# Optimization experiments

Hardware: AMD Instinct MI355X
Metric: run time of the kernel (lower is better)

## Reference

```python
import jax, jax.numpy as jnp
import numpy as np

EPS = 1e-06


def setup_inputs() -> dict:
    key = jax.random.key(0)
    kx, kw, kb = jax.random.split(key, 3)
    C = 128
    x = jax.random.normal(kx, (8, C, 256, 256), dtype=jnp.float32)
    # 1x1 conv weights: [C_out, C_in]
    W = jax.random.normal(kw, (C, C), dtype=jnp.float32) * (1.0 / np.sqrt(C))
    b = jax.random.normal(kb, (C,), dtype=jnp.float32) * 0.01
    return {"x": x, "W": W, "b": b}


def reference(x, W, b):
    # torch.std_mean over channel dim (dim=1), std is unbiased (ddof=1)
    u = jnp.mean(x, axis=1, keepdims=True)                  # [B,1,H,W]
    var = jnp.var(x, axis=1, keepdims=True, ddof=1)         # unbiased
    s = jnp.sqrt(var)
    n_x = (x - u) / (s + EPS)
    # 1x1 conv == pointwise GEMM over channels
    n_x = jnp.einsum('bchw,oc->bohw', n_x, W) + b[None, :, None, None]
    return x * n_x
```

## Files before the change

kernel.cpp:

```cpp
#include <hip/hip_runtime.h>

#define EPS 1e-6f

constexpr int C    = 128;
constexpr int HW   = 65536;
constexpr int TILE = 128;
constexpr int NT   = 512;

typedef __attribute__((ext_vector_type(8))) short bf16x8;
typedef __attribute__((ext_vector_type(4))) float f32x4;

__device__ __forceinline__ unsigned short f2bf(float f) {
    unsigned u = __float_as_uint(f);
    u += 0x7fff + ((u >> 16) & 1);
    return (unsigned short)(u >> 16);
}
__device__ __forceinline__ float bf2f(unsigned short u) {
    return __uint_as_float(((unsigned)u) << 16);
}
__device__ __forceinline__ unsigned pack2(float lo, float hi) {
    return (unsigned)f2bf(lo) | ((unsigned)f2bf(hi) << 16);
}

__global__ __launch_bounds__(NT, 4) void spnorm_kernel(
    const float* __restrict__ x, const float* __restrict__ W,
    const float* __restrict__ bias, float* __restrict__ out)
{
    __shared__ unsigned short buf[TILE * C];
    __shared__ float red1[4][TILE], red2[4][TILE];
    __shared__ float u_s[TILE], iv_s[TILE], se_s[TILE];

    const int tid  = threadIdx.x;
    const int l    = tid & 63;
    const int wv   = tid >> 6;
    const int batch = blockIdx.x >> 9;
    const int hw0   = (blockIdx.x & 511) * TILE;
    const int base  = batch * (C * HW) + hw0;

    const int arow  = (wv << 4) + (l & 15);
    const int acol0 = (l >> 4) << 3;
    bf16x8 afrag[4];
    #pragma unroll
    for (int kk = 0; kk < 4; ++kk) {
        const float* wp = W + arow * C + kk * 32 + acol0;
        float4 wa = *reinterpret_cast<const float4*>(wp);
        float4 wb = *reinterpret_cast<const float4*>(wp + 4);
        bf16x8 f;
        f[0] = (short)f2bf(wa.x); f[1] = (short)f2bf(wa.y);
        f[2] = (short)f2bf(wa.z); f[3] = (short)f2bf(wa.w);
        f[4] = (short)f2bf(wb.x); f[5] = (short)f2bf(wb.y);
        f[6] = (short)f2bf(wb.z); f[7] = (short)f2bf(wb.w);
        afrag[kk] = f;
    }
    const int od = (wv << 4) + ((l >> 4) << 2);
    const f32x4 binit = { bias[od], bias[od + 1], bias[od + 2], bias[od + 3] };

    {
        unsigned short* nb = buf;
        #pragma unroll
        for (int it = 0; it < 8; ++it) {
            int i4 = it * NT + tid;
            int c  = i4 >> 5;
            int p4 = (i4 & 31) << 2;
            float4 v = *reinterpret_cast<const float4*>(x + base + c * HW + p4);
            uint2 d;
            d.x = pack2(v.x, v.y);
            d.y = pack2(v.z, v.w);
            *reinterpret_cast<uint2*>(&nb[c * TILE + p4]) = d;
        }
    }
    __syncthreads();

    const int p = tid & 127;
    const int q = tid >> 7;
    float v[32];
    {
        const unsigned short* nb = buf;
        float s1 = 0.f, s2 = 0.f;
        #pragma unroll
        for (int i = 0; i < 32; ++i) {
            float t = bf2f(nb[(q * 32 + i) * TILE + p]);
            v[i] = t;
            s1 += t;
            s2 = fmaf(t, t, s2);
        }
        red1[q][p] = s1;
        red2[q][p] = s2;
    }
    __syncthreads();
    if (tid < TILE) {
        float s1 = red1[0][tid] + red1[1][tid] + red1[2][tid] + red1[3][tid];
        float s2 = red2[0][tid] + red2[1][tid] + red2[2][tid] + red2[3][tid];
        float u   = s1 * (1.0f / 128.0f);
        float var = fmaxf((s2 - s1 * u) * (1.0f / 127.0f), 0.0f);
        float se  = sqrtf(var) + EPS;
        u_s[tid]  = u;
        se_s[tid] = se;
        iv_s[tid] = 1.0f / se;
    }
    __syncthreads();

    {
        char* nbTc = (char*)buf;
        const float u  = u_s[p];
        const float iv = iv_s[p];
        const int rowoff = p * 256;
        const int swz    = (p & 15) << 4;
        #pragma unroll
        for (int o8 = 0; o8 < 4; ++o8) {
            float n0 = (v[o8 * 8 + 0] - u) * iv;
            float n1 = (v[o8 * 8 + 1] - u) * iv;
            float n2 = (v[o8 * 8 + 2] - u) * iv;
            float n3 = (v[o8 * 8 + 3] - u) * iv;
            float n4 = (v[o8 * 8 + 4] - u) * iv;
            float n5 = (v[o8 * 8 + 5] - u) * iv;
            float n6 = (v[o8 * 8 + 6] - u) * iv;
            float n7 = (v[o8 * 8 + 7] - u) * iv;
            uint4 d;
            d.x = pack2(n0, n1);
            d.y = pack2(n2, n3);
            d.z = pack2(n4, n5);
            d.w = pack2(n6, n7);
            int byte = (rowoff + (q * 4 + o8) * 16) ^ swz;
            *reinterpret_cast<uint4*>(nbTc + byte) = d;
        }
    }
    __syncthreads();

    {
        const char* nbTc = (const char*)buf;
        const int pcol = l & 15;
        const int koff = (l >> 4) << 4;
        const int swz  = pcol << 4;
        float* outp = out + base;
        #pragma unroll
        for (int pt = 0; pt < 8; ++pt) {
            const int pp     = (pt << 4) + pcol;
            const int rowoff = pp * 256;
            f32x4 acc = binit;
            #pragma unroll
            for (int kk = 0; kk < 4; ++kk) {
                int byte = (rowoff + kk * 64 + koff) ^ swz;
                bf16x8 bfrag = *reinterpret_cast<const bf16x8*>(nbTc + byte);
                acc = __builtin_amdgcn_mfma_f32_16x16x32_bf16(afrag[kk], bfrag, acc, 0, 0, 0);
            }
            const float uu = u_s[pp];
            const float se = se_s[pp];
            int nbyte = (rowoff + od * 2) ^ swz;
            uint2 nn = *reinterpret_cast<const uint2*>(nbTc + nbyte);
            float x0 = fmaf(bf2f((unsigned short)(nn.x & 0xffffu)), se, uu);
            float x1 = fmaf(bf2f((unsigned short)(nn.x >> 16)),     se, uu);
            float x2 = fmaf(bf2f((unsigned short)(nn.y & 0xffffu)), se, uu);
            float x3 = fmaf(bf2f((unsigned short)(nn.y >> 16)),     se, uu);
            outp[(od + 0) * HW + pp] = x0 * acc[0];
            outp[(od + 1) * HW + pp] = x1 * acc[1];
            outp[(od + 2) * HW + pp] = x2 * acc[2];
            outp[(od + 3) * HW + pp] = x3 * acc[3];
        }
    }
}

extern "C" void kernel_launch(void* const* d_in, const int* in_sizes, int n_in,
                              void* d_out, int out_size, void* d_ws, size_t ws_size,
                              hipStream_t stream) {
    const float* x = (const float*)d_in[0];
    const float* W = (const float*)d_in[1];
    const float* b = (const float*)d_in[2];
    float* out     = (float*)d_out;

    const int nblk = 8 * HW / TILE;
    spnorm_kernel<<<nblk, NT, 0, stream>>>(x, W, b, out);
}
```

Baseline: 123.4 us.

## Loop each block over eight tiles with register prefetch of the next tile

Each block now processes eight consecutive 128-pixel tiles instead of one, so the grid shrinks eightfold. The next tile's global loads are issued into registers at the start of each iteration and written into a separate LDS input buffer after the normalization stage, overlapping global load latency with the reduction, normalize and MFMA work. A second LDS buffer holds the transposed normalized tile, and full __syncthreads are replaced by lgkmcnt waits plus raw barriers. The larger LDS footprint and the 32 prefetch registers may reduce resident blocks per CU, and the smaller grid leaves less parallelism to hide memory latency.

```diff
diff --git a/kernel.cpp b/kernel.cpp
--- a/kernel.cpp
+++ b/kernel.cpp
@@ -2,10 +2,11 @@
 
 #define EPS 1e-6f
 
-constexpr int C    = 128;
-constexpr int HW   = 65536;
-constexpr int TILE = 128;
-constexpr int NT   = 512;
+constexpr int C      = 128;
+constexpr int HW     = 65536;
+constexpr int TILE   = 128;
+constexpr int NT     = 512;
+constexpr int NTILES = 8;
 
 typedef __attribute__((ext_vector_type(8))) short bf16x8;
 typedef __attribute__((ext_vector_type(4))) float f32x4;
@@ -22,20 +23,34 @@
     return (unsigned)f2bf(lo) | ((unsigned)f2bf(hi) << 16);
 }
 
+#define BAR() do { \
+    asm volatile("s_waitcnt lgkmcnt(0)" ::: "memory"); \
+    __builtin_amdgcn_s_barrier(); \
+    __builtin_amdgcn_sched_barrier(0); \
+} while (0)
+
 __global__ __launch_bounds__(NT, 4) void spnorm_kernel(
     const float* __restrict__ x, const float* __restrict__ W,
     const float* __restrict__ bias, float* __restrict__ out)
 {
-    __shared__ unsigned short buf[TILE * C];
+    __shared__ unsigned short bufN[C * TILE];
+    __shared__ unsigned short bufT[C * TILE];
     __shared__ float red1[4][TILE], red2[4][TILE];
     __shared__ float u_s[TILE], iv_s[TILE], se_s[TILE];
 
-    const int tid  = threadIdx.x;
-    const int l    = tid & 63;
-    const int wv   = tid >> 6;
-    const int batch = blockIdx.x >> 9;
-    const int hw0   = (blockIdx.x & 511) * TILE;
-    const int base  = batch * (C * HW) + hw0;
+    const int tid = threadIdx.x;
+    const int l   = tid & 63;
+    const int wv  = tid >> 6;
+
+    const int blkPerImg = HW / (TILE * NTILES);
+    const int batch = blockIdx.x / blkPerImg;
+    const int hw0   = (blockIdx.x % blkPerImg) * (TILE * NTILES);
+    const int ibase = batch * (C * HW) + hw0;
+
+    const int sc  = tid >> 5;
+    const int sp4 = (tid & 31) << 2;
+    const int p = tid & 127;
+    const int q = tid >> 7;
 
     const int arow  = (wv << 4) + (l & 15);
     const int acol0 = (l >> 4) << 3;
@@ -56,106 +71,120 @@
     const f32x4 binit = { bias[od], bias[od + 1], bias[od + 2], bias[od + 3] };
 
     {
-        unsigned short* nb = buf;
+        const float* xb = x + ibase;
         #pragma unroll
         for (int it = 0; it < 8; ++it) {
-            int i4 = it * NT + tid;
-            int c  = i4 >> 5;
-            int p4 = (i4 & 31) << 2;
-            float4 v = *reinterpret_cast<const float4*>(x + base + c * HW + p4);
+            float4 v = *reinterpret_cast<const float4*>(xb + (it * 16 + sc) * HW + sp4);
             uint2 d;
             d.x = pack2(v.x, v.y);
             d.y = pack2(v.z, v.w);
-            *reinterpret_cast<uint2*>(&nb[c * TILE + p4]) = d;
+            *reinterpret_cast<uint2*>(&bufN[(it * 16 + sc) * TILE + sp4]) = d;
         }
     }
-    __syncthreads();
-
-    const int p = tid & 127;
-    const int q = tid >> 7;
-    float v[32];
-    {
-        const unsigned short* nb = buf;
-        float s1 = 0.f, s2 = 0.f;
-        #pragma unroll
-        for (int i = 0; i < 32; ++i) {
-            float t = bf2f(nb[(q * 32 + i) * TILE + p]);
-            v[i] = t;
-            s1 += t;
-            s2 = fmaf(t, t, s2);
-        }
-        red1[q][p] = s1;
-        red2[q][p] = s2;
-    }
-    __syncthreads();
-    if (tid < TILE) {
-        float s1 = red1[0][tid] + red1[1][tid] + red1[2][tid] + red1[3][tid];
-        float s2 = red2[0][tid] + red2[1][tid] + red2[2][tid] + red2[3][tid];
-        float u   = s1 * (1.0f / 128.0f);
-        float var = fmaxf((s2 - s1 * u) * (1.0f / 127.0f), 0.0f);
-        float se  = sqrtf(var) + EPS;
-        u_s[tid]  = u;
-        se_s[tid] = se;
-        iv_s[tid] = 1.0f / se;
-    }
-    __syncthreads();
-
-    {
-        char* nbTc = (char*)buf;
-        const float u  = u_s[p];
-        const float iv = iv_s[p];
-        const int rowoff = p * 256;
-        const int swz    = (p & 15) << 4;
-        #pragma unroll
-        for (int o8 = 0; o8 < 4; ++o8) {
-            float n0 = (v[o8 * 8 + 0] - u) * iv;
-            float n1 = (v[o8 * 8 + 1] - u) * iv;
-            float n2 = (v[o8 * 8 + 2] - u) * iv;
-            float n3 = (v[o8 * 8 + 3] - u) * iv;
-            float n4 = (v[o8 * 8 + 4] - u) * iv;
-            float n5 = (v[o8 * 8 + 5] - u) * iv;
-            float n6 = (v[o8 * 8 + 6] - u) * iv;
-            float n7 = (v[o8 * 8 + 7] - u) * iv;
-            uint4 d;
-            d.x = pack2(n0, n1);
-            d.y = pack2(n2, n3);
-            d.z = pack2(n4, n5);
-            d.w = pack2(n6, n7);
-            int byte = (rowoff + (q * 4 + o8) * 16) ^ swz;
-            *reinterpret_cast<uint4*>(nbTc + byte) = d;
-        }
-    }
-    __syncthreads();
-
-    {
-        const char* nbTc = (const char*)buf;
-        const int pcol = l & 15;
-        const int koff = (l >> 4) << 4;
-        const int swz  = pcol << 4;
-        float* outp = out + base;
-        #pragma unroll
-        for (int pt = 0; pt < 8; ++pt) {
-            const int pp     = (pt << 4) + pcol;
-            const int rowoff = pp * 256;
-            f32x4 acc = binit;
-            #pragma unroll
-            for (int kk = 0; kk < 4; ++kk) {
-                int byte = (rowoff + kk * 64 + koff) ^ swz;
-                bf16x8 bfrag = *reinterpret_cast<const bf16x8*>(nbTc + byte);
-                acc = __builtin_amdgcn_mfma_f32_16x16x32_bf16(afrag[kk], bfrag, acc, 0, 0, 0);
-            }
-            const float uu = u_s[pp];
-            const float se = se_s[pp];
-            int nbyte = (rowoff + od * 2) ^ swz;
-            uint2 nn = *reinterpret_cast<const uint2*>(nbTc + nbyte);
-            float x0 = fmaf(bf2f((unsigned short)(nn.x & 0xffffu)), se, uu);
-            float x1 = fmaf(bf2f((unsigned short)(nn.x >> 16)),     se, uu);
-            float x2 = fmaf(bf2f((unsigned short)(nn.y & 0xffffu)), se, uu);
-            float x3 = fmaf(bf2f((unsigned short)(nn.y >> 16)),     se, uu);
-            outp[(od + 0) * HW + pp] = x0 * acc[0];
-            outp[(od + 1) * HW + pp] = x1 * acc[1];
-            outp[(od + 2) * HW + pp] = x2 * acc[2];
-            outp[(od + 3) * HW + pp] = x3 * acc[3];
+    BAR();
+
+    for (int t = 0; t < NTILES; ++t) {
+        float4 pf[8];
+        if (t + 1 < NTILES) {
+            const float* xb = x + ibase + (t + 1) * TILE;
+            #pragma unroll
+            for (int it = 0; it < 8; ++it)
+                pf[it] = *reinterpret_cast<const float4*>(xb + (it * 16 + sc) * HW + sp4);
+        }
+
+        float v[32];
+        {
+            float s1 = 0.f, s2 = 0.f;
+            #pragma unroll
+            for (int i = 0; i < 32; ++i) {
+                float tv = bf2f(bufN[(q * 32 + i) * TILE + p]);
+                v[i] = tv;
+                s1 += tv;
+                s2 = fmaf(tv, tv, s2);
+            }
+            red1[q][p] = s1;
+            red2[q][p] = s2;
+        }
+        BAR();
+        if (tid < TILE) {
+            float s1 = red1[0][tid] + red1[1][tid] + red1[2][tid] + red1[3][tid];
+            float s2 = red2[0][tid] + red2[1][tid] + red2[2][tid] + red2[3][tid];
+            float u   = s1 * (1.0f / 128.0f);
+            float var = fmaxf((s2 - s1 * u) * (1.0f / 127.0f), 0.0f);
+            float se  = sqrtf(var) + EPS;
+            u_s[tid]  = u;
+            se_s[tid] = se;
+            iv_s[tid] = 1.0f / se;
+        }
+        BAR();
+
+        {
+            char* tb = (char*)bufT;
+            const float u  = u_s[p];
+            const float iv = iv_s[p];
+            const int rowoff = p * 256;
+            const int swz    = (p & 15) << 4;
+            #pragma unroll
+            for (int o8 = 0; o8 < 4; ++o8) {
+                float n0 = (v[o8 * 8 + 0] - u) * iv;
+                float n1 = (v[o8 * 8 + 1] - u) * iv;
+                float n2 = (v[o8 * 8 + 2] - u) * iv;
+                float n3 = (v[o8 * 8 + 3] - u) * iv;
+                float n4 = (v[o8 * 8 + 4] - u) * iv;
+                float n5 = (v[o8 * 8 + 5] - u) * iv;
+                float n6 = (v[o8 * 8 + 6] - u) * iv;
+                float n7 = (v[o8 * 8 + 7] - u) * iv;
+                uint4 d;
+                d.x = pack2(n0, n1);
+                d.y = pack2(n2, n3);
+                d.z = pack2(n4, n5);
+                d.w = pack2(n6, n7);
+                int byte = (rowoff + (q * 4 + o8) * 16) ^ swz;
+                *reinterpret_cast<uint4*>(tb + byte) = d;
+            }
+        }
+
+        if (t + 1 < NTILES) {
+            #pragma unroll
+            for (int it = 0; it < 8; ++it) {
+                uint2 d;
+                d.x = pack2(pf[it].x, pf[it].y);
+                d.y = pack2(pf[it].z, pf[it].w);
+                *reinterpret_cast<uint2*>(&bufN[(it * 16 + sc) * TILE + sp4]) = d;
+            }
+        }
+        BAR();
+
+        {
+            const char* tb = (const char*)bufT;
+            const int pcol = l & 15;
+            const int koff = (l >> 4) << 4;
+            const int swz  = pcol << 4;
+            float* outp = out + ibase + t * TILE;
+            #pragma unroll
+            for (int pt = 0; pt < 8; ++pt) {
+                const int pp     = (pt << 4) + pcol;
+                const int rowoff = pp * 256;
+                f32x4 acc = binit;
+                #pragma unroll
+                for (int kk = 0; kk < 4; ++kk) {
+                    int byte = (rowoff + kk * 64 + koff) ^ swz;
+                    bf16x8 bfrag = *reinterpret_cast<const bf16x8*>(tb + byte);
+                    acc = __builtin_amdgcn_mfma_f32_16x16x32_bf16(afrag[kk], bfrag, acc, 0, 0, 0);
+                }
+                const float uu = u_s[pp];
+                const float se = se_s[pp];
+                int nbyte = (rowoff + od * 2) ^ swz;
+                uint2 nn = *reinterpret_cast<const uint2*>(tb + nbyte);
+                float x0 = fmaf(bf2f((unsigned short)(nn.x & 0xffffu)), se, uu);
+                float x1 = fmaf(bf2f((unsigned short)(nn.x >> 16)),     se, uu);
+                float x2 = fmaf(bf2f((unsigned short)(nn.y & 0xffffu)), se, uu);
+                float x3 = fmaf(bf2f((unsigned short)(nn.y >> 16)),     se, uu);
+                outp[(od + 0) * HW + pp] = x0 * acc[0];
+                outp[(od + 1) * HW + pp] = x1 * acc[1];
+                outp[(od + 2) * HW + pp] = x2 * acc[2];
+                outp[(od + 3) * HW + pp] = x3 * acc[3];
+            }
         }
     }
 }
@@ -168,6 +197,6 @@
     const float* b = (const float*)d_in[2];
     float* out     = (float*)d_out;
 
-    const int nblk = 8 * HW / TILE;
+    const int nblk = 8 * HW / (TILE * NTILES);
     spnorm_kernel<<<nblk, NT, 0, stream>>>(x, W, b, out);
 }
```

Result: slower. 197.2 us (+59.8%).

## Load x directly into registers and fuse stats reduction to drop staging pass

Applied to the files above, without the earlier changes.

Each thread now reads its 32 channel values of x straight from global memory into registers in full fp32, replacing the bf16 staging buffer in LDS and the second LDS read pass. The reduction is finalized redundantly by all four thread groups, so one __syncthreads and the u/iv shared-memory broadcast are removed. Statistics are now computed from fp32 rather than bf16-rounded values, which improves accuracy. The trade-off is scalar strided 4-byte global loads (coalesced across lanes) instead of float4 loads, plus a little redundant arithmetic.

```diff
diff --git a/kernel.cpp b/kernel.cpp
--- a/kernel.cpp
+++ b/kernel.cpp
@@ -26,16 +26,27 @@
     const float* __restrict__ x, const float* __restrict__ W,
     const float* __restrict__ bias, float* __restrict__ out)
 {
-    __shared__ unsigned short buf[TILE * C];
+    __shared__ unsigned short bufT[C * TILE];
     __shared__ float red1[4][TILE], red2[4][TILE];
-    __shared__ float u_s[TILE], iv_s[TILE], se_s[TILE];
+    __shared__ float u_s[TILE], se_s[TILE];
 
-    const int tid  = threadIdx.x;
-    const int l    = tid & 63;
-    const int wv   = tid >> 6;
+    const int tid = threadIdx.x;
+    const int l   = tid & 63;
+    const int wv  = tid >> 6;
     const int batch = blockIdx.x >> 9;
     const int hw0   = (blockIdx.x & 511) * TILE;
     const int base  = batch * (C * HW) + hw0;
+
+    const int p = tid & 127;
+    const int q = tid >> 7;
+
+    float v[32];
+    {
+        const float* xp = x + base + q * 32 * HW + p;
+        #pragma unroll
+        for (int i = 0; i < 32; ++i)
+            v[i] = xp[i * HW];
+    }
 
     const int arow  = (wv << 4) + (l & 15);
     const int acol0 = (l >> 4) << 3;
@@ -56,54 +67,29 @@
     const f32x4 binit = { bias[od], bias[od + 1], bias[od + 2], bias[od + 3] };
 
     {
-        unsigned short* nb = buf;
-        #pragma unroll
-        for (int it = 0; it < 8; ++it) {
-            int i4 = it * NT + tid;
-            int c  = i4 >> 5;
-            int p4 = (i4 & 31) << 2;
-            float4 v = *reinterpret_cast<const float4*>(x + base + c * HW + p4);
-            uint2 d;
-            d.x = pack2(v.x, v.y);
-            d.y = pack2(v.z, v.w);
-            *reinterpret_cast<uint2*>(&nb[c * TILE + p4]) = d;
-        }
-    }
-    __syncthreads();
-
-    const int p = tid & 127;
-    const int q = tid >> 7;
-    float v[32];
-    {
-        const unsigned short* nb = buf;
         float s1 = 0.f, s2 = 0.f;
         #pragma unroll
         for (int i = 0; i < 32; ++i) {
-            float t = bf2f(nb[(q * 32 + i) * TILE + p]);
-            v[i] = t;
-            s1 += t;
-            s2 = fmaf(t, t, s2);
+            s1 += v[i];
+            s2 = fmaf(v[i], v[i], s2);
         }
         red1[q][p] = s1;
         red2[q][p] = s2;
     }
     __syncthreads();
-    if (tid < TILE) {
-        float s1 = red1[0][tid] + red1[1][tid] + red1[2][tid] + red1[3][tid];
-        float s2 = red2[0][tid] + red2[1][tid] + red2[2][tid] + red2[3][tid];
+
+    {
+        float s1 = red1[0][p] + red1[1][p] + red1[2][p] + red1[3][p];
+        float s2 = red2[0][p] + red2[1][p] + red2[2][p] + red2[3][p];
         float u   = s1 * (1.0f / 128.0f);
         float var = fmaxf((s2 - s1 * u) * (1.0f / 127.0f), 0.0f);
         float se  = sqrtf(var) + EPS;
-        u_s[tid]  = u;
-        se_s[tid] = se;
-        iv_s[tid] = 1.0f / se;
-    }
-    __syncthreads();
-
-    {
-        char* nbTc = (char*)buf;
-        const float u  = u_s[p];
-        const float iv = iv_s[p];
+        float iv  = 1.0f / se;
+        if (q == 0) {
+            u_s[p]  = u;
+            se_s[p] = se;
+        }
+        char* tb = (char*)bufT;
         const int rowoff = p * 256;
         const int swz    = (p & 15) << 4;
         #pragma unroll
@@ -122,13 +108,13 @@
             d.z = pack2(n4, n5);
             d.w = pack2(n6, n7);
             int byte = (rowoff + (q * 4 + o8) * 16) ^ swz;
-            *reinterpret_cast<uint4*>(nbTc + byte) = d;
+            *reinterpret_cast<uint4*>(tb + byte) = d;
         }
     }
     __syncthreads();
 
     {
-        const char* nbTc = (const char*)buf;
+        const char* tb = (const char*)bufT;
         const int pcol = l & 15;
         const int koff = (l >> 4) << 4;
         const int swz  = pcol << 4;
@@ -141,13 +127,13 @@
             #pragma unroll
             for (int kk = 0; kk < 4; ++kk) {
                 int byte = (rowoff + kk * 64 + koff) ^ swz;
-                bf16x8 bfrag = *reinterpret_cast<const bf16x8*>(nbTc + byte);
+                bf16x8 bfrag = *reinterpret_cast<const bf16x8*>(tb + byte);
                 acc = __builtin_amdgcn_mfma_f32_16x16x32_bf16(afrag[kk], bfrag, acc, 0, 0, 0);
             }
             const float uu = u_s[pp];
             const float se = se_s[pp];
             int nbyte = (rowoff + od * 2) ^ swz;
-            uint2 nn = *reinterpret_cast<const uint2*>(nbTc + nbyte);
+            uint2 nn = *reinterpret_cast<const uint2*>(tb + nbyte);
             float x0 = fmaf(bf2f((unsigned short)(nn.x & 0xffffu)), se, uu);
             float x1 = fmaf(bf2f((unsigned short)(nn.x >> 16)),     se, uu);
             float x2 = fmaf(bf2f((unsigned short)(nn.y & 0xffffu)), se, uu);
```

After: 121.3 us. Within noise of the previous version (-1.7%).
